# Optimization experiments

Measured on AMD Instinct MI355X. Metric: run time of the kernel, lower is better.

Reference implementation:

```python
import jax, jax.numpy as jnp
import numpy as np

B, N, DIM = 4, 4096, 512
H, DH, M, ITERS = 8, 64, 256, 6
KW = 33  # residual conv kernel length (along seq)


def setup_inputs() -> dict:
    key = jax.random.key(0)
    k1, k2, k3, k4 = jax.random.split(key, 4)
    return {
        "x": jax.random.normal(k1, (B, N, DIM), dtype=jnp.float32),
        "Wqkv": jax.random.normal(k2, (DIM, 3 * H * DH), dtype=jnp.float32) * 0.02,
        "Wout": jax.random.normal(k3, (H * DH, DIM), dtype=jnp.float32) * 0.02,
        "bout": jnp.zeros((DIM,), dtype=jnp.float32),
        "res_kernel": jax.random.normal(k4, (H, 1, KW, 1), dtype=jnp.float32) * 0.1,
    }


def _pinv_iter(x):
    # Moore-Penrose iterative pseudo-inverse, 6 Newton-Schulz-like steps.
    col = jnp.abs(x).sum(-1)  # ... i
    row = jnp.abs(x).sum(-2)  # ... j
    z = jnp.swapaxes(x, -1, -2) / (jnp.max(col) * jnp.max(row))
    I = jnp.eye(x.shape[-1], dtype=x.dtype)
    for _ in range(ITERS):
        xz = x @ z
        z = 0.25 * z @ (13.0 * I - xz @ (15.0 * I - xz @ (7.0 * I - xz)))
    return z


def reference(x, Wqkv, Wout, bout, res_kernel):
    b, n, _ = x.shape
    l = n // M  # landmark pooling window (n divisible by M -> no padding branch)
    scale = DH ** -0.5

    qkv = x @ Wqkv  # [b, n, 3*h*dh]
    q, k, v = jnp.split(qkv, 3, axis=-1)
    to_bhnd = lambda t: t.reshape(b, n, H, DH).transpose(0, 2, 1, 3)
    q, k, v = to_bhnd(q), to_bhnd(k), to_bhnd(v)
    q = q * scale

    # landmarks: mean over contiguous windows of size l
    q_lm = q.reshape(b, H, M, l, DH).sum(3) / l  # [b,h,m,dh]
    k_lm = k.reshape(b, H, M, l, DH).sum(3) / l

    sim1 = jnp.einsum('bhid,bhjd->bhij', q, k_lm)     # [b,h,n,m]
    sim2 = jnp.einsum('bhid,bhjd->bhij', q_lm, k_lm)  # [b,h,m,m]
    sim3 = jnp.einsum('bhid,bhjd->bhij', q_lm, k)     # [b,h,m,n]

    attn1 = jax.nn.softmax(sim1, axis=-1)
    attn2 = jax.nn.softmax(sim2, axis=-1)
    attn3 = jax.nn.softmax(sim3, axis=-1)

    attn2_inv = _pinv_iter(attn2)
    out = (attn1 @ attn2_inv) @ (attn3 @ v)  # [b,h,n,dh]

    # depthwise residual conv along the sequence axis of v
    pad = KW // 2
    conv = jax.lax.conv_general_dilated(
        v, res_kernel,
        window_strides=(1, 1),
        padding=((pad, pad), (0, 0)),
        dimension_numbers=('NCHW', 'OIHW', 'NCHW'),
        feature_group_count=H,
    )
    out = out + conv

    out = out.transpose(0, 2, 1, 3).reshape(b, n, H * DH)
    return out @ Wout + bout
```

## Files before the change

kernel.cpp:

```cpp
#include <hip/hip_runtime.h>
#include <math.h>

constexpr int BATCH = 4;
constexpr int SEQ   = 4096;
constexpr int DIMC  = 512;
constexpr int NH    = 8;
constexpr int HD    = 64;
constexpr int NLM   = 256;
constexpr int LWIN  = 16;
constexpr int KWIN  = 33;
constexpr int BH    = BATCH * NH;

typedef __attribute__((ext_vector_type(8))) short  bfrag;
typedef __attribute__((ext_vector_type(4))) float  ffrag;
typedef __attribute__((ext_vector_type(8))) unsigned short us8;
typedef __attribute__((ext_vector_type(4))) unsigned short us4;
typedef unsigned short ush;

__device__ __forceinline__ ush f2bf(float f) {
  unsigned u = __builtin_bit_cast(unsigned, f);
  return (ush)((u + 0x7FFFu + ((u >> 16) & 1u)) >> 16);
}
__device__ __forceinline__ float bf2f(ush h) {
  unsigned u = ((unsigned)h) << 16;
  return __builtin_bit_cast(float, u);
}
__device__ __forceinline__ void splitf(float f, ush& h, ush& l) {
  h = f2bf(f);
  l = f2bf(f - bf2f(h));
}
__device__ __forceinline__ void gl_lds16(const ush* g, ush* l) {
  __builtin_amdgcn_global_load_lds(
      (const __attribute__((address_space(1))) void*)g,
      (__attribute__((address_space(3))) void*)l, 16, 0, 0);
}

__global__ void split_flat(const float* __restrict__ src, ush* __restrict__ oh,
                           ush* __restrict__ ol, int n4) {
  for (int i = blockIdx.x * 256 + threadIdx.x; i < n4; i += gridDim.x * 256) {
    float4 f = ((const float4*)src)[i];
    us4 h, l;
    float fs[4] = {f.x, f.y, f.z, f.w};
#pragma unroll
    for (int j = 0; j < 4; ++j) {
      ush hh, ll;
      splitf(fs[j], hh, ll);
      h[j] = hh; l[j] = ll;
    }
    ((us4*)oh)[i] = h;
    ((us4*)ol)[i] = l;
  }
}

__global__ __launch_bounds__(256) void transpose_split_w(const float* __restrict__ in,
                                                         ush* __restrict__ oh,
                                                         ush* __restrict__ ol,
                                                         int R, int C) {
  __shared__ float T[32][33];
  const int tid = threadIdx.x;
  const int c0 = blockIdx.x * 32, r0 = blockIdx.y * 32;
#pragma unroll
  for (int u = 0; u < 4; ++u) {
    int r = (tid >> 5) * 4 + u, cl = tid & 31;
    T[r][cl] = in[(size_t)(r0 + r) * C + c0 + cl];
  }
  __syncthreads();
#pragma unroll
  for (int u = 0; u < 4; ++u) {
    int cl = (tid >> 5) * 4 + u, rl = tid & 31;
    float f = T[rl][cl];
    ush h, l; splitf(f, h, l);
    size_t o = (size_t)(c0 + cl) * R + r0 + rl;
    oh[o] = h; ol[o] = l;
  }
}

__global__ __launch_bounds__(256) void qkv_mfma(const ush* __restrict__ xh,
                                                const ush* __restrict__ xl,
                                                const ush* __restrict__ wTh,
                                                const ush* __restrict__ wTl,
                                                ush* __restrict__ q_bf,
                                                ush* __restrict__ k_bf,
                                                ush* __restrict__ v_bf,
                                                float* __restrict__ qlm,
                                                float* __restrict__ klm) {
  __shared__ ush Ash[128][40], Asl[128][40];
  __shared__ ush Bsh[128][40], Bsl[128][40];
  const int tid = threadIdx.x;
  const int w = tid >> 6, lane = tid & 63;
  const int lm = lane & 15, lq = lane >> 4;
  const int wm = w >> 1, wn = w & 1;
  const int row0 = blockIdx.x * 128, col0 = blockIdx.y * 128;
  const ffrag fz = {0.f, 0.f, 0.f, 0.f};
  ffrag acc[4][4];
#pragma unroll
  for (int i = 0; i < 4; ++i)
#pragma unroll
    for (int j = 0; j < 4; ++j) acc[i][j] = fz;

  const int sm = tid >> 1, skoff = (tid & 1) * 16;
  for (int k0 = 0; k0 < 512; k0 += 32) {
    __syncthreads();
    {
      size_t ao = (size_t)(row0 + sm) * 512 + k0 + skoff;
      *(us8*)&Ash[sm][skoff]     = *(const us8*)&xh[ao];
      *(us8*)&Ash[sm][skoff + 8] = *(const us8*)&xh[ao + 8];
      *(us8*)&Asl[sm][skoff]     = *(const us8*)&xl[ao];
      *(us8*)&Asl[sm][skoff + 8] = *(const us8*)&xl[ao + 8];
      size_t bo = (size_t)(col0 + sm) * 512 + k0 + skoff;
      *(us8*)&Bsh[sm][skoff]     = *(const us8*)&wTh[bo];
      *(us8*)&Bsh[sm][skoff + 8] = *(const us8*)&wTh[bo + 8];
      *(us8*)&Bsl[sm][skoff]     = *(const us8*)&wTl[bo];
      *(us8*)&Bsl[sm][skoff + 8] = *(const us8*)&wTl[bo + 8];
    }
    __syncthreads();
    bfrag ah[4], al[4], bh[4], bl[4];
#pragma unroll
    for (int mt = 0; mt < 4; ++mt) {
      ah[mt] = *(const bfrag*)&Ash[64 * wm + 16 * mt + lm][8 * lq];
      al[mt] = *(const bfrag*)&Asl[64 * wm + 16 * mt + lm][8 * lq];
    }
#pragma unroll
    for (int nt = 0; nt < 4; ++nt) {
      bh[nt] = *(const bfrag*)&Bsh[64 * wn + 16 * nt + lm][8 * lq];
      bl[nt] = *(const bfrag*)&Bsl[64 * wn + 16 * nt + lm][8 * lq];
    }
#pragma unroll
    for (int mt = 0; mt < 4; ++mt)
#pragma unroll
      for (int nt = 0; nt < 4; ++nt) {
        acc[mt][nt] = __builtin_amdgcn_mfma_f32_16x16x32_bf16(ah[mt], bh[nt], acc[mt][nt], 0, 0, 0);
        acc[mt][nt] = __builtin_amdgcn_mfma_f32_16x16x32_bf16(al[mt], bh[nt], acc[mt][nt], 0, 0, 0);
        acc[mt][nt] = __builtin_amdgcn_mfma_f32_16x16x32_bf16(ah[mt], bl[nt], acc[mt][nt], 0, 0, 0);
      }
  }
#pragma unroll
  for (int mt = 0; mt < 4; ++mt) {
    int rbase = row0 + 64 * wm + 16 * mt;
    int b = rbase >> 12;
    int ntok_base = rbase & 4095;
    int win = ntok_base >> 4;
#pragma unroll
    for (int nt = 0; nt < 4; ++nt) {
      int n_local = 64 * wn + 16 * nt;
      int col = col0 + n_local + lm;
      int which = col >> 9;
      int h = (col >> 6) & 7;
      int d = col & 63;
      int bh_i = b * NH + h;
      float scale = (which == 0) ? 0.125f : 1.0f;
      float vals[4];
      float s = 0.f;
#pragma unroll
      for (int r = 0; r < 4; ++r) {
        vals[r] = acc[mt][nt][r] * scale;
        s += vals[r];
      }
      ush* dst = which == 0 ? q_bf : (which == 1 ? k_bf : v_bf);
#pragma unroll
      for (int r = 0; r < 4; ++r) {
        int ntok = ntok_base + 4 * lq + r;
        dst[((size_t)bh_i * SEQ + ntok) * HD + d] = f2bf(vals[r]);
      }
      if (which < 2) {
        s += __shfl_xor(s, 16);
        s += __shfl_xor(s, 32);
        if (lq == 0) {
          float* lmdst = which == 0 ? qlm : klm;
          lmdst[((size_t)bh_i * NLM + win) * HD + d] = s * (1.0f / LWIN);
        }
      }
    }
  }
}

__global__ __launch_bounds__(256) void sim2_softmax(const float* __restrict__ qlm,
                                                    const float* __restrict__ klm,
                                                    ush* __restrict__ a2h,
                                                    ush* __restrict__ a2l) {
  int i = blockIdx.x & 255;
  int bh = blockIdx.x >> 8;
  int j = threadIdx.x;
  __shared__ float qrow[64];
  __shared__ float red[256];
  if (j < 64) qrow[j] = qlm[((size_t)bh * NLM + i) * HD + j];
  __syncthreads();
  const float* kr = klm + ((size_t)bh * NLM + j) * HD;
  float s = 0.f;
#pragma unroll
  for (int d = 0; d < 64; d += 4) {
    float4 kv = *(const float4*)&kr[d];
    s += qrow[d] * kv.x + qrow[d + 1] * kv.y + qrow[d + 2] * kv.z + qrow[d + 3] * kv.w;
  }
  red[j] = s; __syncthreads();
  for (int off = 128; off > 0; off >>= 1) {
    if (j < off) red[j] = fmaxf(red[j], red[j + off]);
    __syncthreads();
  }
  float mx = red[0]; __syncthreads();
  float e = expf(s - mx);
  red[j] = e; __syncthreads();
  for (int off = 128; off > 0; off >>= 1) {
    if (j < off) red[j] += red[j + off];
    __syncthreads();
  }
  float val = e / red[0];
  size_t o = ((size_t)bh * NLM + i) * NLM + j;
  ush h, l; splitf(val, h, l);
  a2h[o] = h; a2l[o] = l;
}

__global__ __launch_bounds__(256) void colmax(const ush* __restrict__ a2h,
                                              float* __restrict__ red) {
  int bh = blockIdx.x;
  int t = threadIdx.x;
  const size_t base = (size_t)bh * NLM * NLM;
  float cs = 0.f;
  for (int i = 0; i < NLM; ++i) cs += bf2f(a2h[base + (size_t)i * NLM + t]);
  __shared__ float r1[256];
  r1[t] = cs; __syncthreads();
  for (int off = 128; off > 0; off >>= 1) {
    if (t < off) r1[t] = fmaxf(r1[t], r1[t + off]);
    __syncthreads();
  }
  if (t == 0) red[bh] = r1[0];
}

__global__ void finalize_scale(float* __restrict__ red) {
  if (threadIdx.x == 0) {
    float m1 = -1e30f;
    for (int i = 0; i < BH; ++i) m1 = fmaxf(m1, red[i]);
    red[64] = 1.0f / m1;
  }
}

__global__ __launch_bounds__(256) void zinit_split(const ush* __restrict__ a2h,
                                                   const ush* __restrict__ a2l,
                                                   const float* __restrict__ red,
                                                   ush* __restrict__ zAh, ush* __restrict__ zAl,
                                                   ush* __restrict__ zBh, ush* __restrict__ zBl) {
  __shared__ float T[32][33];
  const int tid = threadIdx.x;
  const int bh = blockIdx.z;
  const int j0 = blockIdx.x * 32, i0 = blockIdx.y * 32;
  const float s = red[64];
  const size_t base = (size_t)bh * NLM * NLM;
#pragma unroll
  for (int u = 0; u < 4; ++u) {
    int jl = (tid >> 5) * 4 + u, il = tid & 31;
    size_t o = base + (size_t)(j0 + jl) * NLM + i0 + il;
    float a = (bf2f(a2h[o]) + bf2f(a2l[o])) * s;
    T[jl][il] = a;
    ush h, l; splitf(a, h, l);
    zBh[o] = h; zBl[o] = l;
  }
  __syncthreads();
#pragma unroll
  for (int u = 0; u < 4; ++u) {
    int il = (tid >> 5) * 4 + u, jl = tid & 31;
    float a = T[jl][il];
    ush h, l; splitf(a, h, l);
    size_t o = base + (size_t)(i0 + il) * NLM + j0 + jl;
    zAh[o] = h; zAl[o] = l;
  }
}

__device__ __forceinline__ void stage_gemm(
    ush (*S)[2][8][64][8],
    const ush* Ah, const ush* Al, const ush* Bh, const ush* Bl,
    const ush* E1h, const ush* E1l, const ush* E2h, const ush* E2l,
    ush* oAh, ush* oAl, ush* oBh, ush* oBl,
    int M, int N, int K, float alpha, float beta, float coef,
    int bx, int by, int batch, int tid) {
  const size_t abase = (size_t)batch * M * K;
  const size_t bbase = (size_t)batch * N * K;
  const size_t ebase = (size_t)batch * M * N;
  const int w = tid >> 6, lane = tid & 63;
  const int lm = lane & 15, lq = lane >> 4;
  const int wm = w >> 1, wn = w & 1;
  const int row0 = bx * 64, col0 = by * 64;
  const bool uAl = (Al != nullptr);
  const bool uBl = (Bl != nullptr);
  const ffrag fz = {0.f, 0.f, 0.f, 0.f};
  ffrag acc[2][2] = {{fz, fz}, {fz, fz}};

  const size_t arow = abase + (size_t)(row0 + lane) * K;
  const size_t brow = bbase + (size_t)(col0 + lane) * K;

  for (int k0 = 0; k0 < K; k0 += 64) {
    __syncthreads();
#pragma unroll
    for (int ci = 0; ci < 2; ++ci) {
      int c = 2 * w + ci;
      gl_lds16(&Ah[arow + k0 + 8 * c], &S[0][0][c][0][0]);
      gl_lds16(&Bh[brow + k0 + 8 * c], &S[1][0][c][0][0]);
      if (uAl) gl_lds16(&Al[arow + k0 + 8 * c], &S[0][1][c][0][0]);
      if (uBl) gl_lds16(&Bl[brow + k0 + 8 * c], &S[1][1][c][0][0]);
    }
    __syncthreads();
#pragma unroll
    for (int ks = 0; ks < 2; ++ks) {
      bfrag ah[2], al[2], bhf[2], blf[2];
#pragma unroll
      for (int mt = 0; mt < 2; ++mt) {
        ah[mt] = *(const bfrag*)&S[0][0][4 * ks + lq][32 * wm + 16 * mt + lm][0];
        if (uAl) al[mt] = *(const bfrag*)&S[0][1][4 * ks + lq][32 * wm + 16 * mt + lm][0];
      }
#pragma unroll
      for (int nt = 0; nt < 2; ++nt) {
        bhf[nt] = *(const bfrag*)&S[1][0][4 * ks + lq][32 * wn + 16 * nt + lm][0];
        if (uBl) blf[nt] = *(const bfrag*)&S[1][1][4 * ks + lq][32 * wn + 16 * nt + lm][0];
      }
#pragma unroll
      for (int mt = 0; mt < 2; ++mt)
#pragma unroll
        for (int nt = 0; nt < 2; ++nt) {
          acc[mt][nt] = __builtin_amdgcn_mfma_f32_16x16x32_bf16(ah[mt], bhf[nt], acc[mt][nt], 0, 0, 0);
          if (uAl) acc[mt][nt] = __builtin_amdgcn_mfma_f32_16x16x32_bf16(al[mt], bhf[nt], acc[mt][nt], 0, 0, 0);
          if (uBl) acc[mt][nt] = __builtin_amdgcn_mfma_f32_16x16x32_bf16(ah[mt], blf[nt], acc[mt][nt], 0, 0, 0);
        }
    }
  }
#pragma unroll
  for (int mt = 0; mt < 2; ++mt)
#pragma unroll
    for (int nt = 0; nt < 2; ++nt) {
      int n = col0 + 32 * wn + 16 * nt + lm;
#pragma unroll
      for (int r = 0; r < 4; ++r) {
        int m = row0 + 32 * wm + 16 * mt + 4 * lq + r;
        float c = acc[mt][nt][r];
        float e = 0.f;
        size_t eo = ebase + (size_t)m * N + n;
        if (E1h) {
          float t = bf2f(E1h[eo]);
          if (E1l) t += bf2f(E1l[eo]);
          e += alpha * t;
        }
        if (E2h) {
          float t = bf2f(E2h[eo]);
          if (E2l) t += bf2f(E2l[eo]);
          e += beta * t;
        }
        float y = coef * (e - c);
        ush h, l; splitf(y, h, l);
        if (oAh) {
          size_t o = ebase + (size_t)m * N + n;
          oAh[o] = h;
          if (oAl) oAl[o] = l;
        }
        if (oBh) {
          size_t o = (size_t)batch * N * M + (size_t)n * M + m;
          oBh[o] = h;
          if (oBl) oBl[o] = l;
        }
      }
    }
}

__global__ __launch_bounds__(256) void bgemm_split(
    const ush* Ah, const ush* Al, const ush* Bh, const ush* Bl,
    const ush* E1h, const ush* E1l, const ush* E2h, const ush* E2l,
    ush* oAh, ush* oAl, ush* oBh, ush* oBl,
    int M, int N, int K, float alpha, float beta, float coef) {
  __shared__ ush S[2][2][8][64][8];
  stage_gemm(S, Ah, Al, Bh, Bl, E1h, E1l, E2h, E2l, oAh, oAl, oBh, oBl,
             M, N, K, alpha, beta, coef, blockIdx.x, blockIdx.y, blockIdx.z,
             threadIdx.x);
}

__global__ __launch_bounds__(256) void ns_s2(
    const ush* Yh, const ush* Yl, const ush* zh, const ush* zl,
    ush* t2h, ush* t2l, ush* Uh, ush* Ul) {
  __shared__ ush S[2][2][8][64][8];
  const int bz = blockIdx.z, batch = bz >> 1;
  if ((bz & 1) == 0) {
    stage_gemm(S, Yh, Yl, Yh, Yl, Yh, Yl, nullptr, nullptr,
               t2h, t2l, nullptr, nullptr,
               256, 256, 256, 7.f, 0.f, 1.f,
               blockIdx.x, blockIdx.y, batch, threadIdx.x);
  } else {
    stage_gemm(S, zh, zl, Yh, Yl, nullptr, nullptr, nullptr, nullptr,
               Uh, Ul, nullptr, nullptr,
               256, 256, 256, 0.f, 0.f, -1.f,
               blockIdx.x, blockIdx.y, batch, threadIdx.x);
  }
}

__global__ __launch_bounds__(256) void vT_cvt_bf(const ush* __restrict__ v_bf,
                                                 ush* __restrict__ vT) {
  __shared__ ush T[64][72];
  const int bh = blockIdx.y;
  const int n0 = blockIdx.x * 64;
  const int tid = threadIdx.x;
  {
    int n = tid >> 2, off = (tid & 3) * 16;
    const ush* src = &v_bf[((size_t)bh * SEQ + n0 + n) * HD + off];
    *(us8*)&T[n][off] = *(const us8*)src;
    *(us8*)&T[n][off + 8] = *(const us8*)&src[8];
  }
  __syncthreads();
  {
    int d = tid >> 2, noff = (tid & 3) * 16;
    us8 o0, o1;
#pragma unroll
    for (int j = 0; j < 8; ++j) o0[j] = T[noff + j][d];
#pragma unroll
    for (int j = 0; j < 8; ++j) o1[j] = T[noff + 8 + j][d];
    ush* dst = &vT[((size_t)bh * HD + d) * SEQ + n0 + noff];
    *(us8*)dst = o0;
    *(us8*)&dst[8] = o1;
  }
}

constexpr int NCH = 4;
__global__ __launch_bounds__(256) void sim3_mfma(const float* __restrict__ qlm,
                                                 const ush* __restrict__ k_bf,
                                                 const ush* __restrict__ vT_bf,
                                                 float* __restrict__ O_part,
                                                 float* __restrict__ l_part) {
  constexpr int CHUNK = SEQ / NCH;
  __shared__ ush Qs[64][72];
  __shared__ ush Ks[128][72];
  __shared__ ush Vs[64][136];
  __shared__ ush Ps[64][136];
  const int bh = blockIdx.z;
  const int m0 = blockIdx.x * 64;
  const int n_base = blockIdx.y * CHUNK;
  const int tid = threadIdx.x;
  const int w = tid >> 6, lane = tid & 63;
  const int lm = lane & 15, lq = lane >> 4;
  {
    int m = tid >> 2, off = (tid & 3) * 16;
    const float* src = &qlm[((size_t)bh * NLM + m0 + m) * HD + off];
    us8 o0, o1;
#pragma unroll
    for (int j = 0; j < 8; ++j) o0[j] = f2bf(src[j]);
#pragma unroll
    for (int j = 0; j < 8; ++j) o1[j] = f2bf(src[8 + j]);
    *(us8*)&Qs[m][off] = o0;
    *(us8*)&Qs[m][off + 8] = o1;
  }
  const ffrag fz = {0.f, 0.f, 0.f, 0.f};
  ffrag O[4] = {fz, fz, fz, fz};
  float lsum[4] = {0.f, 0.f, 0.f, 0.f};

  for (int n0 = 0; n0 < CHUNK; n0 += 128) {
    __syncthreads();
    {
      int n = tid >> 1, off = (tid & 1) * 32;
      const ush* src = &k_bf[((size_t)bh * SEQ + n_base + n0 + n) * HD + off];
#pragma unroll
      for (int u = 0; u < 4; ++u) *(us8*)&Ks[n][off + 8 * u] = *(const us8*)&src[8 * u];
    }
    {
      int d = tid >> 2, off = (tid & 3) * 32;
      const ush* src = &vT_bf[((size_t)bh * HD + d) * SEQ + n_base + n0 + off];
#pragma unroll
      for (int u = 0; u < 4; ++u) *(us8*)&Vs[d][off + 8 * u] = *(const us8*)&src[8 * u];
    }
    __syncthreads();
    ffrag S[8] = {fz, fz, fz, fz, fz, fz, fz, fz};
#pragma unroll
    for (int ks = 0; ks < 2; ++ks) {
      bfrag a = *(const bfrag*)&Qs[16 * w + lm][32 * ks + 8 * lq];
#pragma unroll
      for (int t = 0; t < 8; ++t) {
        bfrag b = *(const bfrag*)&Ks[16 * t + lm][32 * ks + 8 * lq];
        S[t] = __builtin_amdgcn_mfma_f32_16x16x32_bf16(a, b, S[t], 0, 0, 0);
      }
    }
#pragma unroll
    for (int t = 0; t < 8; ++t)
#pragma unroll
      for (int r = 0; r < 4; ++r) {
        float p = __expf(S[t][r]);
        lsum[r] += p;
        Ps[16 * w + 4 * lq + r][16 * t + lm] = f2bf(p);
      }
    __syncthreads();
#pragma unroll
    for (int kk = 0; kk < 4; ++kk) {
      bfrag a = *(const bfrag*)&Ps[16 * w + lm][32 * kk + 8 * lq];
#pragma unroll
      for (int t2 = 0; t2 < 4; ++t2) {
        bfrag b = *(const bfrag*)&Vs[16 * t2 + lm][32 * kk + 8 * lq];
        O[t2] = __builtin_amdgcn_mfma_f32_16x16x32_bf16(a, b, O[t2], 0, 0, 0);
      }
    }
  }
#pragma unroll
  for (int r = 0; r < 4; ++r) {
#pragma unroll
    for (int off = 1; off < 16; off <<= 1) lsum[r] += __shfl_xor(lsum[r], off);
  }
  const size_t pbase = (size_t)blockIdx.y * 32 + bh;
  if (lm == 0) {
#pragma unroll
    for (int r = 0; r < 4; ++r)
      l_part[pbase * NLM + m0 + 16 * w + 4 * lq + r] = lsum[r];
  }
#pragma unroll
  for (int t2 = 0; t2 < 4; ++t2)
#pragma unroll
    for (int r = 0; r < 4; ++r) {
      int m = m0 + 16 * w + 4 * lq + r;
      int d = 16 * t2 + lm;
      O_part[(pbase * NLM + m) * HD + d] = O[t2][r];
    }
}

__global__ __launch_bounds__(256) void sim3_finalize(const float* __restrict__ O_part,
                                                     const float* __restrict__ l_part,
                                                     ush* __restrict__ svBh,
                                                     ush* __restrict__ svBl) {
  __shared__ float T[128][17];
  __shared__ float ls[128];
  const int bh = blockIdx.y;
  const int d0 = (blockIdx.x & 3) * 16;
  const int m0 = (blockIdx.x >> 2) * 128;
  const int tid = threadIdx.x;
  if (tid < 128) {
    float s = 0.f;
#pragma unroll
    for (int c = 0; c < NCH; ++c) s += l_part[(size_t)(c * 32 + bh) * NLM + m0 + tid];
    ls[tid] = s;
  }
#pragma unroll
  for (int i = 0; i < 8; ++i) {
    int e = i * 256 + tid;
    int m = e >> 4, dd = e & 15;
    float s = 0.f;
#pragma unroll
    for (int c = 0; c < NCH; ++c)
      s += O_part[(((size_t)(c * 32 + bh)) << 14) + (size_t)(m0 + m) * HD + d0 + dd];
    T[m][dd] = s;
  }
  __syncthreads();
#pragma unroll
  for (int i = 0; i < 8; ++i) {
    int e = i * 256 + tid;
    int dd = e >> 7, m = e & 127;
    float val = T[m][dd] / ls[m];
    ush h, l; splitf(val, h, l);
    size_t o = ((size_t)bh * HD + d0 + dd) * NLM + m0 + m;
    svBh[o] = h; svBl[o] = l;
  }
}

__global__ __launch_bounds__(256) void attn1_mfma(const ush* __restrict__ q_bf,
                                                  const float* __restrict__ klm,
                                                  const ush* __restrict__ ttT,
                                                  float* __restrict__ outp) {
  __shared__ ush bufA[256 * 72];
  __shared__ ush bufB[64 * 264];
  const int bh = blockIdx.y;
  const int b = bh >> 3, h = bh & 7;
  const int i0 = blockIdx.x * 64;
  const int tid = threadIdx.x;
  const int w = tid >> 6, lane = tid & 63;
  const int lm = lane & 15, lq = lane >> 4;
  {
    int m = tid >> 2, off = (tid & 3) * 16;
    const ush* src = &q_bf[((size_t)bh * SEQ + i0 + m) * HD + off];
    *(us8*)&bufB[m * 72 + off] = *(const us8*)src;
    *(us8*)&bufB[m * 72 + off + 8] = *(const us8*)&src[8];
  }
  {
    const float* kb = klm + (size_t)bh * NLM * HD;
#pragma unroll
    for (int u = 0; u < 16; ++u) {
      int e4 = u * 256 + tid;
      float4 f = ((const float4*)kb)[e4];
      int row = e4 >> 4, col = (e4 & 15) * 4;
      ush* p = &bufA[row * 72 + col];
      p[0] = f2bf(f.x); p[1] = f2bf(f.y); p[2] = f2bf(f.z); p[3] = f2bf(f.w);
    }
  }
  __syncthreads();
  const ffrag fz = {0.f, 0.f, 0.f, 0.f};
  ffrag S[16];
#pragma unroll
  for (int t = 0; t < 16; ++t) S[t] = fz;
#pragma unroll
  for (int ks = 0; ks < 2; ++ks) {
    bfrag a = *(const bfrag*)&bufB[(16 * w + lm) * 72 + 32 * ks + 8 * lq];
#pragma unroll
    for (int t = 0; t < 16; ++t) {
      bfrag bb = *(const bfrag*)&bufA[(16 * t + lm) * 72 + 32 * ks + 8 * lq];
      S[t] = __builtin_amdgcn_mfma_f32_16x16x32_bf16(a, bb, S[t], 0, 0, 0);
    }
  }
  float rinv[4];
  float ev[16][4];
#pragma unroll
  for (int r = 0; r < 4; ++r) {
    float mx = -INFINITY;
#pragma unroll
    for (int t = 0; t < 16; ++t) mx = fmaxf(mx, S[t][r]);
#pragma unroll
    for (int off = 1; off < 16; off <<= 1) mx = fmaxf(mx, __shfl_xor(mx, off));
    float sm = 0.f;
#pragma unroll
    for (int t = 0; t < 16; ++t) { ev[t][r] = __expf(S[t][r] - mx); sm += ev[t][r]; }
#pragma unroll
    for (int off = 1; off < 16; off <<= 1) sm += __shfl_xor(sm, off);
    rinv[r] = 1.0f / sm;
  }
  __syncthreads();
#pragma unroll
  for (int t = 0; t < 16; ++t)
#pragma unroll
    for (int r = 0; r < 4; ++r)
      bufB[(16 * w + 4 * lq + r) * 264 + 16 * t + lm] = f2bf(ev[t][r]);
  {
    const ush* tb = ttT + (size_t)bh * HD * NLM;
#pragma unroll
    for (int u = 0; u < 8; ++u) {
      int e8 = u * 256 + tid;
      int row = e8 >> 5, col = (e8 & 31) * 8;
      *(us8*)&bufA[row * 264 + col] = *(const us8*)&tb[row * NLM + col];
    }
  }
  __syncthreads();
  ffrag O[4] = {fz, fz, fz, fz};
#pragma unroll
  for (int kk = 0; kk < 8; ++kk) {
    bfrag a = *(const bfrag*)&bufB[(16 * w + lm) * 264 + 32 * kk + 8 * lq];
#pragma unroll
    for (int t2 = 0; t2 < 4; ++t2) {
      bfrag bb = *(const bfrag*)&bufA[(16 * t2 + lm) * 264 + 32 * kk + 8 * lq];
      O[t2] = __builtin_amdgcn_mfma_f32_16x16x32_bf16(a, bb, O[t2], 0, 0, 0);
    }
  }
#pragma unroll
  for (int t2 = 0; t2 < 4; ++t2)
#pragma unroll
    for (int r = 0; r < 4; ++r) {
      int i = i0 + 16 * w + 4 * lq + r;
      int d = 16 * t2 + lm;
      outp[((size_t)b * SEQ + i) * DIMC + h * HD + d] = O[t2][r] * rinv[r];
    }
}

__global__ __launch_bounds__(256) void conv_add_split(const float* __restrict__ outp,
                                                      const ush* __restrict__ vT,
                                                      const float* __restrict__ kern,
                                                      ush* __restrict__ oh,
                                                      ush* __restrict__ ol) {
  __shared__ float vt[64 * 97];
  __shared__ float ks[KWIN];
  const int bh = blockIdx.y;
  const int b = bh >> 3, hh = bh & 7;
  const int n0 = blockIdx.x * 64;
  const int tid = threadIdx.x;
  if (tid < KWIN) ks[tid] = kern[hh * KWIN + tid];
  for (int e = tid; e < 64 * 96; e += 256) {
    int d = e / 96, c = e % 96;
    int n = n0 - 16 + c;
    vt[d * 97 + c] = (n >= 0 && n < SEQ) ? bf2f(vT[((size_t)bh * HD + d) * SEQ + n]) : 0.f;
  }
  __syncthreads();
  const int d = tid & 63, g = tid >> 6;
  float wreg[48];
#pragma unroll
  for (int j = 0; j < 48; ++j) wreg[j] = vt[d * 97 + g * 16 + j];
#pragma unroll
  for (int nn = 0; nn < 16; ++nn) {
    float s = 0.f;
#pragma unroll
    for (int t = 0; t < KWIN; ++t) s = fmaf(ks[t], wreg[nn + t], s);
    int n = n0 + g * 16 + nn;
    size_t o = ((size_t)b * SEQ + n) * DIMC + hh * HD + d;
    float val = outp[o] + s;
    ush h, l; splitf(val, h, l);
    oh[o] = h; ol[o] = l;
  }
}

__global__ __launch_bounds__(256) void out_gemm_split(const ush* __restrict__ ah_g,
                                                      const ush* __restrict__ al_g,
                                                      const ush* __restrict__ bh_g,
                                                      const ush* __restrict__ bl_g,
                                                      const float* __restrict__ bias,
                                                      float* __restrict__ out) {
  __shared__ ush Ash[128][40], Asl[128][40];
  __shared__ ush Bsh[128][40], Bsl[128][40];
  const int tid = threadIdx.x;
  const int w = tid >> 6, lane = tid & 63;
  const int lm = lane & 15, lq = lane >> 4;
  const int wm = w >> 1, wn = w & 1;
  const int row0 = blockIdx.x * 128, col0 = blockIdx.y * 128;
  const ffrag fz = {0.f, 0.f, 0.f, 0.f};
  ffrag acc[4][4];
#pragma unroll
  for (int i = 0; i < 4; ++i)
#pragma unroll
    for (int j = 0; j < 4; ++j) acc[i][j] = fz;

  const int sm = tid >> 1, skoff = (tid & 1) * 16;
  for (int k0 = 0; k0 < 512; k0 += 32) {
    __syncthreads();
    {
      size_t ao = (size_t)(row0 + sm) * 512 + k0 + skoff;
      *(us8*)&Ash[sm][skoff]     = *(const us8*)&ah_g[ao];
      *(us8*)&Ash[sm][skoff + 8] = *(const us8*)&ah_g[ao + 8];
      *(us8*)&Asl[sm][skoff]     = *(const us8*)&al_g[ao];
      *(us8*)&Asl[sm][skoff + 8] = *(const us8*)&al_g[ao + 8];
      size_t bo = (size_t)(col0 + sm) * 512 + k0 + skoff;
      *(us8*)&Bsh[sm][skoff]     = *(const us8*)&bh_g[bo];
      *(us8*)&Bsh[sm][skoff + 8] = *(const us8*)&bh_g[bo + 8];
      *(us8*)&Bsl[sm][skoff]     = *(const us8*)&bl_g[bo];
      *(us8*)&Bsl[sm][skoff + 8] = *(const us8*)&bl_g[bo + 8];
    }
    __syncthreads();
    bfrag ah[4], al[4], bh[4], bl[4];
#pragma unroll
    for (int mt = 0; mt < 4; ++mt) {
      ah[mt] = *(const bfrag*)&Ash[64 * wm + 16 * mt + lm][8 * lq];
      al[mt] = *(const bfrag*)&Asl[64 * wm + 16 * mt + lm][8 * lq];
    }
#pragma unroll
    for (int nt = 0; nt < 4; ++nt) {
      bh[nt] = *(const bfrag*)&Bsh[64 * wn + 16 * nt + lm][8 * lq];
      bl[nt] = *(const bfrag*)&Bsl[64 * wn + 16 * nt + lm][8 * lq];
    }
#pragma unroll
    for (int mt = 0; mt < 4; ++mt)
#pragma unroll
      for (int nt = 0; nt < 4; ++nt) {
        acc[mt][nt] = __builtin_amdgcn_mfma_f32_16x16x32_bf16(ah[mt], bh[nt], acc[mt][nt], 0, 0, 0);
        acc[mt][nt] = __builtin_amdgcn_mfma_f32_16x16x32_bf16(al[mt], bh[nt], acc[mt][nt], 0, 0, 0);
        acc[mt][nt] = __builtin_amdgcn_mfma_f32_16x16x32_bf16(ah[mt], bl[nt], acc[mt][nt], 0, 0, 0);
      }
  }
#pragma unroll
  for (int mt = 0; mt < 4; ++mt)
#pragma unroll
    for (int nt = 0; nt < 4; ++nt) {
      int n = col0 + 64 * wn + 16 * nt + lm;
      float bv = bias[n];
#pragma unroll
      for (int r = 0; r < 4; ++r) {
        int m = row0 + 64 * wm + 16 * mt + 4 * lq + r;
        out[(size_t)m * 512 + n] = acc[mt][nt][r] + bv;
      }
    }
}

extern "C" void kernel_launch(void* const* d_in, const int* in_sizes, int n_in,
                              void* d_out, int out_size, void* d_ws, size_t ws_size,
                              hipStream_t stream) {
  const float* x    = (const float*)d_in[0];
  const float* Wqkv = (const float*)d_in[1];
  const float* Wout = (const float*)d_in[2];
  const float* bout = (const float*)d_in[3];
  const float* rker = (const float*)d_in[4];
  float* out = (float*)d_out;
  float* ws = (float*)d_ws;

  ush*   v_bf   = (ush*)(ws);
  ush*   q_bf   = (ush*)(ws + 4194304);
  float* regA   = ws + 8388608;
  float* regB   = ws + 16777216;
  float* qlm    = ws + 25165824;
  float* klm    = ws + 25690112;
  float* regC   = ws + 26214400;
  float* a2reg  = ws + 28311552;
  float* zAreg  = ws + 30408704;
  float* zBreg  = ws + 34603008;
  float* xzreg  = ws + 38797312;
  float* t3reg  = ws + 43515904;
  float* wqkvT  = ws + 45613056;
  float* woutT  = ws + 46399488;
  float* red    = ws + 46661632;

  ush* k_bf  = (ush*)regA;
  float* outp = regA;
  ush* xh = (ush*)regB;
  ush* xl = (ush*)(regB + 4194304);
  ush* outph = (ush*)regB;
  ush* outpl = (ush*)(regB + 4194304);
  ush* a2h = (ush*)a2reg;
  ush* a2l = (ush*)(a2reg + 1048576);
  ush* zA_[4] = {(ush*)zAreg, (ush*)(zAreg + 1048576), (ush*)(zAreg + 2097152), (ush*)(zAreg + 3145728)};
  ush* zB_[4] = {(ush*)zBreg, (ush*)(zBreg + 1048576), (ush*)(zBreg + 2097152), (ush*)(zBreg + 3145728)};
  ush* Y_h  = (ush*)xzreg;
  ush* Y_l  = (ush*)(xzreg + 1048576);
  ush* t2_h = (ush*)regC;
  ush* t2_l = (ush*)(regC + 1048576);
  ush* U_h  = (ush*)t3reg;
  ush* U_l  = (ush*)(t3reg + 1048576);
  ush* vT_bf = (ush*)zBreg;
  float* O_part = xzreg;
  float* l_part = xzreg + 2097152;
  ush* svB_h = (ush*)t3reg;
  ush* svB_l = (ush*)(t3reg + 262144);
  ush* ttT   = (ush*)regC;
  ush* wqkvT_h = (ush*)wqkvT;
  ush* wqkvT_l = (ush*)(wqkvT + 393216);
  ush* woutT_h = (ush*)woutT;
  ush* woutT_l = (ush*)(woutT + 131072);

  split_flat<<<2048, 256, 0, stream>>>(x, xh, xl, 2097152);
  transpose_split_w<<<dim3(48, 16), 256, 0, stream>>>(Wqkv, wqkvT_h, wqkvT_l, 512, 1536);
  transpose_split_w<<<dim3(16, 16), 256, 0, stream>>>(Wout, woutT_h, woutT_l, 512, 512);

  qkv_mfma<<<dim3(128, 12), 256, 0, stream>>>(xh, xl, wqkvT_h, wqkvT_l,
                                              q_bf, k_bf, v_bf, qlm, klm);

  sim2_softmax<<<8192, 256, 0, stream>>>(qlm, klm, a2h, a2l);
  colmax<<<32, 256, 0, stream>>>(a2h, red);
  finalize_scale<<<1, 64, 0, stream>>>(red);
  zinit_split<<<dim3(8, 8, 32), 256, 0, stream>>>(a2h, a2l, red,
                                                  zA_[0], zA_[1], zA_[2], zA_[3]);

  ush** zc = zA_;
  ush** zn = zB_;
  for (int it = 0; it < 6; ++it) {
    const bool zin_s  = (it == 5);
    const bool a2_s   = (it >= 4);
    const bool mid_s  = (it >= 4);
    const bool zout_s = (it >= 4);
    bgemm_split<<<dim3(4, 4, 32), 256, 0, stream>>>(
        a2h, a2_s ? a2l : nullptr,
        zc[2], zin_s ? zc[3] : nullptr,
        nullptr, nullptr, nullptr, nullptr,
        Y_h, mid_s ? Y_l : nullptr, nullptr, nullptr,
        256, 256, 256, 0.f, 0.f, -1.f);
    ns_s2<<<dim3(4, 4, 64), 256, 0, stream>>>(
        Y_h, mid_s ? Y_l : nullptr,
        zc[0], zin_s ? zc[1] : nullptr,
        t2_h, mid_s ? t2_l : nullptr,
        U_h, mid_s ? U_l : nullptr);
    bgemm_split<<<dim3(4, 4, 32), 256, 0, stream>>>(
        U_h, mid_s ? U_l : nullptr,
        t2_h, mid_s ? t2_l : nullptr,
        zc[0], zin_s ? zc[1] : nullptr,
        U_h, mid_s ? U_l : nullptr,
        zn[0], zout_s ? zn[1] : nullptr,
        zn[2], zout_s ? zn[3] : nullptr,
        256, 256, 256, -13.f, 15.f, -0.25f);
    ush** tp = zc; zc = zn; zn = tp;
  }

  vT_cvt_bf<<<dim3(64, 32), 256, 0, stream>>>(v_bf, vT_bf);
  sim3_mfma<<<dim3(4, NCH, 32), 256, 0, stream>>>(qlm, k_bf, vT_bf, O_part, l_part);
  sim3_finalize<<<dim3(8, 32), 256, 0, stream>>>(O_part, l_part, svB_h, svB_l);

  bgemm_split<<<dim3(4, 1, 32), 256, 0, stream>>>(
      zc[0], zc[1], svB_h, svB_l,
      nullptr, nullptr, nullptr, nullptr,
      nullptr, nullptr, ttT, nullptr, 256, 64, 256, 0.f, 0.f, -1.f);

  attn1_mfma<<<dim3(64, 32), 256, 0, stream>>>(q_bf, klm, ttT, outp);
  conv_add_split<<<dim3(64, 32), 256, 0, stream>>>(outp, vT_bf, rker, outph, outpl);
  out_gemm_split<<<dim3(128, 4), 256, 0, stream>>>(outph, outpl, woutT_h, woutT_l, bout, out);
}
```

Measured before the change: 739.8 us.

## Drop weight low-part MFMA in QKV GEMM and write V transposed directly

Measured after the change: 714.2 us. -3.5%, faster.

```diff
diff --git a/kernel.cpp b/kernel.cpp
--- a/kernel.cpp
+++ b/kernel.cpp
@@ -78,14 +78,13 @@
 __global__ __launch_bounds__(256) void qkv_mfma(const ush* __restrict__ xh,
                                                 const ush* __restrict__ xl,
                                                 const ush* __restrict__ wTh,
-                                                const ush* __restrict__ wTl,
                                                 ush* __restrict__ q_bf,
                                                 ush* __restrict__ k_bf,
-                                                ush* __restrict__ v_bf,
+                                                ush* __restrict__ vT,
                                                 float* __restrict__ qlm,
                                                 float* __restrict__ klm) {
   __shared__ ush Ash[128][40], Asl[128][40];
-  __shared__ ush Bsh[128][40], Bsl[128][40];
+  __shared__ ush Bsh[128][40];
   const int tid = threadIdx.x;
   const int w = tid >> 6, lane = tid & 63;
   const int lm = lane & 15, lq = lane >> 4;
@@ -110,28 +109,23 @@
       size_t bo = (size_t)(col0 + sm) * 512 + k0 + skoff;
       *(us8*)&Bsh[sm][skoff]     = *(const us8*)&wTh[bo];
       *(us8*)&Bsh[sm][skoff + 8] = *(const us8*)&wTh[bo + 8];
-      *(us8*)&Bsl[sm][skoff]     = *(const us8*)&wTl[bo];
-      *(us8*)&Bsl[sm][skoff + 8] = *(const us8*)&wTl[bo + 8];
-    }
-    __syncthreads();
-    bfrag ah[4], al[4], bh[4], bl[4];
+    }
+    __syncthreads();
+    bfrag ah[4], al[4], bh[4];
 #pragma unroll
     for (int mt = 0; mt < 4; ++mt) {
       ah[mt] = *(const bfrag*)&Ash[64 * wm + 16 * mt + lm][8 * lq];
       al[mt] = *(const bfrag*)&Asl[64 * wm + 16 * mt + lm][8 * lq];
     }
 #pragma unroll
-    for (int nt = 0; nt < 4; ++nt) {
+    for (int nt = 0; nt < 4; ++nt)
       bh[nt] = *(const bfrag*)&Bsh[64 * wn + 16 * nt + lm][8 * lq];
-      bl[nt] = *(const bfrag*)&Bsl[64 * wn + 16 * nt + lm][8 * lq];
-    }
 #pragma unroll
     for (int mt = 0; mt < 4; ++mt)
 #pragma unroll
       for (int nt = 0; nt < 4; ++nt) {
         acc[mt][nt] = __builtin_amdgcn_mfma_f32_16x16x32_bf16(ah[mt], bh[nt], acc[mt][nt], 0, 0, 0);
         acc[mt][nt] = __builtin_amdgcn_mfma_f32_16x16x32_bf16(al[mt], bh[nt], acc[mt][nt], 0, 0, 0);
-        acc[mt][nt] = __builtin_amdgcn_mfma_f32_16x16x32_bf16(ah[mt], bl[nt], acc[mt][nt], 0, 0, 0);
       }
   }
 #pragma unroll
@@ -156,13 +150,17 @@
         vals[r] = acc[mt][nt][r] * scale;
         s += vals[r];
       }
-      ush* dst = which == 0 ? q_bf : (which == 1 ? k_bf : v_bf);
-#pragma unroll
-      for (int r = 0; r < 4; ++r) {
-        int ntok = ntok_base + 4 * lq + r;
-        dst[((size_t)bh_i * SEQ + ntok) * HD + d] = f2bf(vals[r]);
-      }
-      if (which < 2) {
+      if (which == 2) {
+        ush* dst = &vT[((size_t)bh_i * HD + d) * SEQ + ntok_base + 4 * lq];
+#pragma unroll
+        for (int r = 0; r < 4; ++r) dst[r] = f2bf(vals[r]);
+      } else {
+        ush* dst = which == 0 ? q_bf : k_bf;
+#pragma unroll
+        for (int r = 0; r < 4; ++r) {
+          int ntok = ntok_base + 4 * lq + r;
+          dst[((size_t)bh_i * SEQ + ntok) * HD + d] = f2bf(vals[r]);
+        }
         s += __shfl_xor(s, 16);
         s += __shfl_xor(s, 32);
         if (lq == 0) {
@@ -387,32 +385,6 @@
   }
 }
 
-__global__ __launch_bounds__(256) void vT_cvt_bf(const ush* __restrict__ v_bf,
-                                                 ush* __restrict__ vT) {
-  __shared__ ush T[64][72];
-  const int bh = blockIdx.y;
-  const int n0 = blockIdx.x * 64;
-  const int tid = threadIdx.x;
-  {
-    int n = tid >> 2, off = (tid & 3) * 16;
-    const ush* src = &v_bf[((size_t)bh * SEQ + n0 + n) * HD + off];
-    *(us8*)&T[n][off] = *(const us8*)src;
-    *(us8*)&T[n][off + 8] = *(const us8*)&src[8];
-  }
-  __syncthreads();
-  {
-    int d = tid >> 2, noff = (tid & 3) * 16;
-    us8 o0, o1;
-#pragma unroll
-    for (int j = 0; j < 8; ++j) o0[j] = T[noff + j][d];
-#pragma unroll
-    for (int j = 0; j < 8; ++j) o1[j] = T[noff + 8 + j][d];
-    ush* dst = &vT[((size_t)bh * HD + d) * SEQ + n0 + noff];
-    *(us8*)dst = o0;
-    *(us8*)&dst[8] = o1;
-  }
-}
-
 constexpr int NCH = 4;
 __global__ __launch_bounds__(256) void sim3_mfma(const float* __restrict__ qlm,
                                                  const ush* __restrict__ k_bf,
@@ -759,7 +731,7 @@
   float* out = (float*)d_out;
   float* ws = (float*)d_ws;
 
-  ush*   v_bf   = (ush*)(ws);
+  ush*   vT     = (ush*)(ws);
   ush*   q_bf   = (ush*)(ws + 4194304);
   float* regA   = ws + 8388608;
   float* regB   = ws + 16777216;
@@ -791,7 +763,6 @@
   ush* t2_l = (ush*)(regC + 1048576);
   ush* U_h  = (ush*)t3reg;
   ush* U_l  = (ush*)(t3reg + 1048576);
-  ush* vT_bf = (ush*)zBreg;
   float* O_part = xzreg;
   float* l_part = xzreg + 2097152;
   ush* svB_h = (ush*)t3reg;
@@ -806,8 +777,8 @@
   transpose_split_w<<<dim3(48, 16), 256, 0, stream>>>(Wqkv, wqkvT_h, wqkvT_l, 512, 1536);
   transpose_split_w<<<dim3(16, 16), 256, 0, stream>>>(Wout, woutT_h, woutT_l, 512, 512);
 
-  qkv_mfma<<<dim3(128, 12), 256, 0, stream>>>(xh, xl, wqkvT_h, wqkvT_l,
-                                              q_bf, k_bf, v_bf, qlm, klm);
+  qkv_mfma<<<dim3(128, 12), 256, 0, stream>>>(xh, xl, wqkvT_h,
+                                              q_bf, k_bf, vT, qlm, klm);
 
   sim2_softmax<<<8192, 256, 0, stream>>>(qlm, klm, a2h, a2l);
   colmax<<<32, 256, 0, stream>>>(a2h, red);
@@ -844,8 +815,7 @@
     ush** tp = zc; zc = zn; zn = tp;
   }
 
-  vT_cvt_bf<<<dim3(64, 32), 256, 0, stream>>>(v_bf, vT_bf);
-  sim3_mfma<<<dim3(4, NCH, 32), 256, 0, stream>>>(qlm, k_bf, vT_bf, O_part, l_part);
+  sim3_mfma<<<dim3(4, NCH, 32), 256, 0, stream>>>(qlm, k_bf, vT, O_part, l_part);
   sim3_finalize<<<dim3(8, 32), 256, 0, stream>>>(O_part, l_part, svB_h, svB_l);
 
   bgemm_split<<<dim3(4, 1, 32), 256, 0, stream>>>(
@@ -854,6 +824,6 @@
       nullptr, nullptr, ttT, nullptr, 256, 64, 256, 0.f, 0.f, -1.f);
 
   attn1_mfma<<<dim3(64, 32), 256, 0, stream>>>(q_bf, klm, ttT, outp);
-  conv_add_split<<<dim3(64, 32), 256, 0, stream>>>(outp, vT_bf, rker, outph, outpl);
+  conv_add_split<<<dim3(64, 32), 256, 0, stream>>>(outp, vT, rker, outph, outpl);
   out_gemm_split<<<dim3(128, 4), 256, 0, stream>>>(outph, outpl, woutT_h, woutT_l, bout, out);
 }
```
